# Kernel tuning notes

Measured on AMD Instinct MI355X. Metric: run time of the kernel, lower is better.

Reference implementation:

```python
import jax, jax.numpy as jnp
import numpy as np

N, E, D, H, C = 50000, 250000, 300, 4, 75  # nodes, edges, in_size=300, heads=4, out=75 (H*C=300)


def setup_inputs() -> dict:
    key = jax.random.key(0)
    ks = jax.random.split(key, 32)
    rn = lambda k, shape, s=0.05: jax.random.normal(k, shape, jnp.float32) * s
    inp = {}
    inp['x'] = rn(ks[0], (N, D), 1.0)
    inp['edge_index'] = jax.random.randint(ks[1], (2, E), 0, N, dtype=jnp.int32)
    inp['edge_attr'] = rn(ks[2], (E, 4), 1.0)
    inp['obj_normals'] = rn(ks[3], (N, 3), 1.0)
    # parameters (Linear stored as [in, out] so y = x @ W + b)
    inp['Wq'] = rn(ks[4], (D, H * C)); inp['bq'] = rn(ks[5], (H * C,))
    inp['Wk'] = rn(ks[6], (D, H * C)); inp['bk'] = rn(ks[7], (H * C,))
    inp['Wv'] = rn(ks[8], (D, H * C)); inp['bv'] = rn(ks[9], (H * C,))
    inp['We'] = rn(ks[10], (D, H * C))               # lin_edge, no bias
    inp['Wn'] = rn(ks[11], (3, D)); inp['bn'] = rn(ks[12], (D,))      # map_normal
    inp['Wxy'] = rn(ks[13], (2, D)); inp['bxy'] = rn(ks[14], (D,))    # map_xy_relative_coord
    inp['Wloc'] = rn(ks[15], (3 * D, D)); inp['bloc'] = rn(ks[16], (D,))  # map_back_edge_loc
    inp['Wobj'] = rn(ks[17], (2 * D, D)); inp['bobj'] = rn(ks[18], (D,))  # map_back_edge_obj
    inp['Wfus'] = rn(ks[19], (2 * D, D)); inp['bfus'] = rn(ks[20], (D,))  # hv_words_fusion
    inp['Wcls'] = rn(ks[21], (D, 5)); inp['bcls'] = rn(ks[22], (5,))      # horizontal_word_cls
    inp['Wskip'] = rn(ks[23], (D, H * C)); inp['bskip'] = rn(ks[24], (H * C,))  # lin_skip
    inp['vocab'] = rn(ks[25], (7, D), 1.0)  # spatial_vocab_we
    return inp


def reference(x, edge_index, edge_attr, obj_normals,
              Wq, bq, Wk, bk, Wv, bv, We, Wn, bn, Wxy, bxy,
              Wloc, bloc, Wobj, bobj, Wfus, bfus, Wcls, bcls,
              Wskip, bskip, vocab):
    src, dst = edge_index[0], edge_index[1]  # x_j = x[src], x_i = x[dst]
    x_i = x[dst]
    x_j = x[src]
    q = (x_i @ Wq + bq).reshape(E, H, C)
    k = (x_j @ Wk + bk).reshape(E, H, C)
    # vertical (top/bottom) word embeddings gated by edge_attr signs
    top = (edge_attr[:, 0] > 0).astype(x.dtype)[:, None] * vocab[0][None, :]
    bot = (edge_attr[:, 1] < 0).astype(x.dtype)[:, None] * vocab[1][None, :]
    vert = top + bot                                           # [E, D]
    # horizontal word probabilities from geometry + feature cues
    ni = obj_normals[dst] @ Wn + bn
    nj = obj_normals[src] @ Wn + bn
    xy = edge_attr[:, 2:4] @ Wxy + bxy
    loc = jnp.concatenate([xy, ni, nj], axis=1) @ Wloc + bloc
    obj = jnp.concatenate([x_i, x_j - x_i], axis=1) @ Wobj + bobj
    prob = jax.nn.softmax(jnp.tanh(obj + loc) @ Wcls + bcls, axis=1)   # [E, 5]
    horiz = prob @ vocab[2:7]                                  # [E, D]
    edge_word = jnp.concatenate([vert, horiz], axis=1) @ Wfus + bfus   # [E, D]
    ef = (edge_word @ We).reshape(E, H, C)                     # lin_edge
    k = k + ef
    # scaled dot-product attention with per-destination-node softmax
    alpha = (q * k).sum(-1) / jnp.asarray(np.sqrt(C), x.dtype)  # [E, H]
    m = jax.ops.segment_max(alpha, dst, num_segments=N)
    alpha = jnp.exp(alpha - m[dst])
    den = jax.ops.segment_sum(alpha, dst, num_segments=N)
    alpha = alpha / den[dst]
    v = (x_j @ Wv + bv).reshape(E, H, C) + ef
    msg = v * alpha[..., None]                                  # [E, H, C]
    out = jax.ops.segment_sum(msg, dst, num_segments=N).reshape(N, H * C)
    out = out + x @ Wskip + bskip                               # concat heads + root skip
    return out
```

## Files before the change

### kernel.cpp

```cpp
#include <hip/hip_runtime.h>
#include <hip/hip_bf16.h>
#include <math.h>

#define NDIM 300
#define KPAD 320
#define NREAL 1800
#define NPAD 1920

typedef __hip_bfloat16 bf16;
typedef __attribute__((ext_vector_type(8))) short short8;
typedef __attribute__((ext_vector_type(4))) float f32x4;

__device__ __forceinline__ void gl_lds16(const void* g, void* l) {
    __builtin_amdgcn_global_load_lds(
        (const __attribute__((address_space(1))) void*)g,
        (__attribute__((address_space(3))) void*)l, 16, 0, 0);
}

__global__ void small_pre(
    const float* __restrict__ Wn, const float* __restrict__ bn,
    const float* __restrict__ Wxy, const float* __restrict__ bxy,
    const float* __restrict__ Wloc, const float* __restrict__ bloc,
    const float* __restrict__ bobj,
    const float* __restrict__ Wfus,
    const float* __restrict__ vocab,
    float* __restrict__ Wn1, float* __restrict__ Wn2,
    float* __restrict__ Mxy, float* __restrict__ bgeo,
    float* __restrict__ vf5, float* __restrict__ t0, float* __restrict__ t1)
{
    int i = blockIdx.x * blockDim.x + threadIdx.x;
    if (i < 900) {
        int r = i / 300, c = i % 300;
        float s = 0.f;
        for (int k = 0; k < 300; k++) s += Wn[r*300+k] * Wloc[(300+k)*300+c];
        Wn1[i] = s;
    } else if (i < 1800) {
        int j = i - 900; int r = j/300, c = j%300;
        float s = 0.f;
        for (int k = 0; k < 300; k++) s += Wn[r*300+k] * Wloc[(600+k)*300+c];
        Wn2[j] = s;
    } else if (i < 2400) {
        int j = i - 1800; int r = j/300, c = j%300;
        float s = 0.f;
        for (int k = 0; k < 300; k++) s += Wxy[r*300+k] * Wloc[k*300+c];
        Mxy[j] = 2.f * s;
    } else if (i < 2700) {
        int c = i - 2400;
        float s = bloc[c] + bobj[c];
        for (int k = 0; k < 300; k++) s += bxy[k] * Wloc[k*300+c];
        for (int k = 0; k < 300; k++) s += bn[k] * (Wloc[(300+k)*300+c] + Wloc[(600+k)*300+c]);
        bgeo[c] = 2.f * s;
    } else if (i < 4200) {
        int j = i - 2700; int p = j/300, c = j%300;
        float s = 0.f;
        for (int k = 0; k < 300; k++) s += vocab[(2+p)*300+k] * Wfus[(300+k)*300+c];
        vf5[j] = s;
    } else if (i < 4500) {
        int c = i - 4200;
        float s = 0.f;
        for (int k = 0; k < 300; k++) s += vocab[k] * Wfus[k*300+c];
        t0[c] = s;
    } else if (i < 4800) {
        int c = i - 4500;
        float s = 0.f;
        for (int k = 0; k < 300; k++) s += vocab[300+k] * Wfus[k*300+c];
        t1[c] = s;
    }
}

__global__ void small_pre2(
    const float* __restrict__ We, const float* __restrict__ bfus,
    const float* __restrict__ vf5, const float* __restrict__ t0, const float* __restrict__ t1,
    const float* __restrict__ Wcls,
    float* __restrict__ E8, float* __restrict__ WclsT)
{
    int i = blockIdx.x * blockDim.x + threadIdx.x;
    if (i < 2400) {
        int r = i / 300, c = i % 300;
        const float* src;
        if (r == 0) src = t0;
        else if (r == 1) src = t1;
        else if (r == 7) src = bfus;
        else src = vf5 + (r - 2) * 300;
        float s = 0.f;
        for (int k = 0; k < 300; k++) s += src[k] * We[k*300+c];
        E8[i] = s;
    } else if (i < 3900) {
        int j = i - 2400; int cl = j / 300, c = j % 300;
        WclsT[cl * 300 + c] = Wcls[c * 5 + cl];
    }
}

__global__ void pack_w(
    const float* __restrict__ Wq, const float* __restrict__ Wk,
    const float* __restrict__ Wv, const float* __restrict__ Wskip,
    const float* __restrict__ Wobj,
    const float* __restrict__ Wn1, const float* __restrict__ Wn2,
    const float* __restrict__ bq, const float* __restrict__ bk,
    const float* __restrict__ bv, const float* __restrict__ bskip,
    bf16* __restrict__ WcatT, float* __restrict__ bcat)
{
    int i = blockIdx.x * blockDim.x + threadIdx.x;
    if (i < NREAL) {
        int seg = i / 300, jj = i % 300;
        float b = 0.f;
        if (seg == 0) b = bq[jj]; else if (seg == 1) b = bk[jj];
        else if (seg == 2) b = bv[jj]; else if (seg == 3) b = bskip[jj];
        bcat[i] = b;
    }
    if (i < NPAD * KPAD) {
        int c = i / KPAD, k = i % KPAD;
        float v = 0.f;
        if (c < NREAL) {
            int seg = c / 300, jj = c % 300;
            if (k < 300) {
                switch (seg) {
                    case 0: v = Wq[k*300+jj]; break;
                    case 1: v = Wk[k*300+jj]; break;
                    case 2: v = Wv[k*300+jj]; break;
                    case 3: v = Wskip[k*300+jj]; break;
                    case 4: v = Wobj[k*300+jj] - Wobj[(300+k)*300+jj]; break;
                    default: v = Wobj[(300+k)*300+jj]; break;
                }
            } else if (k < 303) {
                if (seg == 4) v = Wn1[(k-300)*300+jj];
                else if (seg == 5) v = Wn2[(k-300)*300+jj];
            }
            if (seg >= 4) v *= 2.f;
        }
        WcatT[i] = __float2bfloat16(v);
    }
}

__global__ void conv_xb(const float* __restrict__ X, const float* __restrict__ Nrm,
                        bf16* __restrict__ Xb, int M)
{
    int i = blockIdx.x * blockDim.x + threadIdx.x;
    int row = i / 40, c8 = i % 40;
    if (row >= M) return;
    int c0 = c8 * 8;
    union { bf16 h[8]; short8 s; } u;
    #pragma unroll
    for (int t = 0; t < 8; t++) {
        int c = c0 + t;
        float v = 0.f;
        if (c < 300)      v = X[(size_t)row * 300 + c];
        else if (c < 303) v = Nrm[(size_t)row * 3 + (c - 300)];
        u.h[t] = __float2bfloat16(v);
    }
    *(short8*)&Xb[(size_t)row * 320 + c0] = u.s;
}

__global__ __launch_bounds__(256) void qe8_k(
    const bf16* __restrict__ Q, const float* __restrict__ E8,
    float* __restrict__ QE8f, int N)
{
    __shared__ bf16 Qs[64 * 300];
    const int tid = threadIdx.x;
    const int n0 = blockIdx.x * 64;
    const int nrows = min(64, N - n0);
    const int ndw = nrows * 150;
    const uint* src = (const uint*)(Q + (size_t)n0 * 300);
    uint* dst = (uint*)Qs;
    for (int i = tid; i < ndw; i += 256) dst[i] = src[i];
    __syncthreads();
    const int w = tid >> 6, l = tid & 63;
    if (l >= nrows) return;
    float acc[8] = {0.f,0.f,0.f,0.f,0.f,0.f,0.f,0.f};
    const int cb = 75 * w;
    for (int cc = 0; cc < 75; cc++) {
        int c = cb + cc;
        float qv = __bfloat162float(Qs[l * 300 + c]);
        #pragma unroll
        for (int s = 0; s < 8; s++) acc[s] += qv * E8[s * 300 + c];
    }
    float* out = QE8f + (size_t)(n0 + l) * 32;
    #pragma unroll
    for (int s = 0; s < 8; s++) out[s * 4 + w] = acc[s];
}

__global__ void hist_k(const int* __restrict__ ei, int* __restrict__ deg, int E) {
    int e = blockIdx.x * blockDim.x + threadIdx.x;
    if (e < E) atomicAdd(&deg[ei[E + e]], 1);
}

__global__ __launch_bounds__(1024) void scan_local(
    const int* __restrict__ deg, int* __restrict__ off, int* __restrict__ bsum, int N)
{
    __shared__ int buf[1024];
    int i = blockIdx.x * 1024 + threadIdx.x;
    int v = (i < N) ? deg[i] : 0;
    buf[threadIdx.x] = v;
    __syncthreads();
    #pragma unroll
    for (int ofs = 1; ofs < 1024; ofs <<= 1) {
        int t = (threadIdx.x >= ofs) ? buf[threadIdx.x - ofs] : 0;
        __syncthreads();
        buf[threadIdx.x] += t;
        __syncthreads();
    }
    if (i < N) off[i] = buf[threadIdx.x] - v;
    if (threadIdx.x == 1023) bsum[blockIdx.x] = buf[1023];
}

__global__ __launch_bounds__(1024) void scan_bsum(
    const int* __restrict__ bsum, int* __restrict__ bexc, int nb)
{
    __shared__ int buf[1024];
    int v = (threadIdx.x < nb) ? bsum[threadIdx.x] : 0;
    buf[threadIdx.x] = v;
    __syncthreads();
    #pragma unroll
    for (int ofs = 1; ofs < 1024; ofs <<= 1) {
        int t = (threadIdx.x >= ofs) ? buf[threadIdx.x - ofs] : 0;
        __syncthreads();
        buf[threadIdx.x] += t;
        __syncthreads();
    }
    if (threadIdx.x < nb) bexc[threadIdx.x] = buf[threadIdx.x] - v;
}

__global__ void scan_add(int* __restrict__ off, int* __restrict__ cur,
                         const int* __restrict__ bexc, int N, int E)
{
    int i = blockIdx.x * blockDim.x + threadIdx.x;
    if (i < N) {
        int o = off[i] + bexc[i >> 10];
        off[i] = o; cur[i] = o;
    }
    if (i == 0) off[N] = E;
}

__global__ void scatter_k(const int* __restrict__ ei, const float* __restrict__ ea,
                          int* __restrict__ cur,
                          int* __restrict__ esrc, int* __restrict__ edst,
                          float* __restrict__ eas, int E) {
    int e = blockIdx.x * blockDim.x + threadIdx.x;
    if (e < E) {
        int s = ei[e];
        int d = ei[E + e];
        float4 a = *(const float4*)&ea[(size_t)e * 4];
        int p = atomicAdd(&cur[d], 1);
        esrc[p] = s;
        edst[p] = d;
        *(float4*)&eas[(size_t)p * 4] = a;
    }
}

__global__ __launch_bounds__(256) void gemm_mfma(
    const bf16* __restrict__ Xb,
    const bf16* __restrict__ Bt, const float* __restrict__ bcat,
    bf16* __restrict__ Q, bf16* __restrict__ Kf, bf16* __restrict__ V,
    float* __restrict__ Ot, bf16* __restrict__ Pi, bf16* __restrict__ Pj,
    int M)
{
    __shared__ __align__(16) bf16 As[2][128 * 32];
    __shared__ __align__(16) bf16 Bs[2][128 * 32];

    const int tid  = threadIdx.x;
    const int wave = tid >> 6;
    const int lane = tid & 63;
    const int r0 = blockIdx.y * 128;
    const int c0 = blockIdx.x * 128;
    const int wm = (wave >> 1) * 64;
    const int wn = (wave & 1) * 64;
    const int lr = lane & 15;
    const int lq = lane >> 4;

    f32x4 acc[4][4];
    #pragma unroll
    for (int j = 0; j < 4; j++)
        #pragma unroll
        for (int i = 0; i < 4; i++) acc[j][i] = (f32x4){0.f, 0.f, 0.f, 0.f};

    const int bcol_l = lane >> 2;
    const int bkp    = (lane & 3) * 8;

    auto stage = [&](int buf, int kb) {
        #pragma unroll
        for (int h = 0; h < 2; h++) {
            int tbase = h * 256 + wave * 64;
            int t = tbase + lane;
            int grow = min(r0 + (t >> 2), M - 1);
            gl_lds16(Xb + (size_t)grow * 320 + kb + (t & 3) * 8,
                     &As[buf][tbase * 8]);
        }
        #pragma unroll
        for (int h = 0; h < 2; h++) {
            int cloc = wave * 32 + h * 16;
            gl_lds16(Bt + (size_t)(c0 + cloc + bcol_l) * KPAD + kb + bkp,
                     &Bs[buf][cloc * 32]);
        }
    };

    stage(0, 0);
    #pragma unroll
    for (int it = 0; it < 10; it++) {
        __syncthreads();
        if (it < 9) stage((it + 1) & 1, (it + 1) * 32);
        const int b = it & 1;
        short8 af[4], bfr[4];
        #pragma unroll
        for (int i = 0; i < 4; i++)
            af[i] = *(const short8*)&As[b][(wm + i * 16 + lr) * 32 + lq * 8];
        #pragma unroll
        for (int j = 0; j < 4; j++)
            bfr[j] = *(const short8*)&Bs[b][(wn + j * 16 + lr) * 32 + lq * 8];
        #pragma unroll
        for (int j = 0; j < 4; j++)
            #pragma unroll
            for (int i = 0; i < 4; i++)
                acc[j][i] = __builtin_amdgcn_mfma_f32_16x16x32_bf16(
                    bfr[j], af[i], acc[j][i], 0, 0, 0);
    }

    #pragma unroll
    for (int j = 0; j < 4; j++) {
        int colb = c0 + wn + j * 16 + lq * 4;
        if (colb >= NREAL) continue;
        int seg = colb / 300, jj = colb - seg * 300;
        float4 bb = *(const float4*)&bcat[colb];
        #pragma unroll
        for (int i = 0; i < 4; i++) {
            int row = r0 + wm + i * 16 + lr;
            if (row >= M) continue;
            float v0 = acc[j][i][0] + bb.x;
            float v1 = acc[j][i][1] + bb.y;
            float v2 = acc[j][i][2] + bb.z;
            float v3 = acc[j][i][3] + bb.w;
            size_t idx = (size_t)row * 300 + jj;
            if (seg == 3) {
                *(float4*)&Ot[idx] = make_float4(v0, v1, v2, v3);
            } else {
                union { bf16 h[4]; uint2 u2; } p;
                p.h[0] = __float2bfloat16(v0); p.h[1] = __float2bfloat16(v1);
                p.h[2] = __float2bfloat16(v2); p.h[3] = __float2bfloat16(v3);
                bf16* base = (seg == 0) ? Q : (seg == 1) ? Kf : (seg == 2) ? V
                           : (seg == 4) ? Pi : Pj;
                *(uint2*)&base[idx] = p.u2;
            }
        }
    }
}

__global__ __launch_bounds__(256) void edge_alpha(
    const int* __restrict__ esrc, const int* __restrict__ edst,
    const float* __restrict__ eas,
    const bf16* __restrict__ Q, const bf16* __restrict__ Kf,
    const bf16* __restrict__ Pi, const bf16* __restrict__ Pj,
    const float* __restrict__ Mxy, const float* __restrict__ bgeo,
    const float* __restrict__ QE8f, const float* __restrict__ WclsT,
    const float* __restrict__ bcls,
    float* __restrict__ Aex, float* __restrict__ W8o,
    int E, int nwaves)
{
    __shared__ float red[4][20 * 68];
    __shared__ float res[4][20];
    const int wv   = threadIdx.x >> 6;
    const int lane = threadIdx.x & 63;
    float* __restrict__ rw = red[wv];
    float* __restrict__ rs = res[wv];
    const int gw  = blockIdx.x * 4 + wv;
    const int per = (E + nwaves - 1) / nwaves;
    const int t0  = gw * per;
    if (t0 >= E) return;
    const int t1 = min(t0 + per, E);

    float mx0[5], mx1[5], bg[5], wcl[5][5];
    #pragma unroll
    for (int r = 0; r < 5; r++) {
        int c = lane + 64 * r;
        bool ok = c < 300;
        mx0[r] = ok ? Mxy[c]       : 0.f;
        mx1[r] = ok ? Mxy[300 + c] : 0.f;
        bg[r]  = ok ? bgeo[c]      : 0.f;
        #pragma unroll
        for (int cl = 0; cl < 5; cl++)
            wcl[cl][r] = ok ? WclsT[cl * 300 + c] : 0.f;
    }
    float bc[5];
    #pragma unroll
    for (int cl = 0; cl < 5; cl++) bc[cl] = bcls[cl];
    const float isc = 0.11547005383792516f;

    for (int t = t0; t < t1; t += 2) {
        const int i0 = t;
        const int i1 = (t + 1 < t1) ? t + 1 : t;
        const int s20 = esrc[i0], s21 = esrc[i1];
        const int d20 = edst[i0], d21 = edst[i1];
        const float4 a40 = *(const float4*)&eas[(size_t)4 * i0];
        const float4 a41 = *(const float4*)&eas[(size_t)4 * i1];

        float prt[18];
        #pragma unroll
        for (int u = 0; u < 2; u++) {
            const int ss = u ? s21 : s20;
            const int dd = u ? d21 : d20;
            const float az = u ? a41.z : a40.z;
            const float aw = u ? a41.w : a40.w;
            const size_t sr = (size_t)ss * 300, dr = (size_t)dd * 300;
            float qv[5], kv[5], tt[5];
            #pragma unroll
            for (int r = 0; r < 5; r++) {
                int c = lane + 64 * r;
                bool ok = c < 300;
                float pi_ = ok ? __bfloat162float(Pi[dr + c]) : 0.f;
                float pj_ = ok ? __bfloat162float(Pj[sr + c]) : 0.f;
                qv[r] = ok ? __bfloat162float(Q [dr + c]) : 0.f;
                kv[r] = ok ? __bfloat162float(Kf[sr + c]) : 0.f;
                float v = pi_ + pj_ + az * mx0[r] + aw * mx1[r] + bg[r];
                tt[r] = fmaf(-2.f, __builtin_amdgcn_rcpf(1.f + __expf(v)), 1.f);
            }
            #pragma unroll
            for (int cl = 0; cl < 5; cl++)
                prt[u * 9 + cl] = tt[0]*wcl[cl][0] + tt[1]*wcl[cl][1] + tt[2]*wcl[cl][2]
                                + tt[3]*wcl[cl][3] + tt[4]*wcl[cl][4];
            float h0 = qv[0] * kv[0];
            float h3 = qv[4] * kv[4];
            float p1 = qv[1] * kv[1], p2 = qv[2] * kv[2], p3 = qv[3] * kv[3];
            float h1 = 0.f, h2 = 0.f;
            if (lane + 64  < 75)  h0 += p1; else h1 += p1;
            if (lane + 128 < 150) h1 += p2; else h2 += p2;
            if (lane + 192 < 225) h2 += p3; else h3 += p3;
            prt[u * 9 + 5] = h0; prt[u * 9 + 6] = h1;
            prt[u * 9 + 7] = h2; prt[u * 9 + 8] = h3;
        }
        #pragma unroll
        for (int v = 0; v < 18; v++) rw[v * 68 + lane] = prt[v];
        #pragma unroll
        for (int i = 0; i < 5; i++) {
            int v = 4 * i + (lane >> 4);
            const f32x4 q4 = *(const f32x4*)&rw[v * 68 + (lane & 15) * 4];
            float s = (q4[0] + q4[1]) + (q4[2] + q4[3]);
            s += __shfl_xor(s, 1, 64);
            s += __shfl_xor(s, 2, 64);
            s += __shfl_xor(s, 4, 64);
            s += __shfl_xor(s, 8, 64);
            if ((lane & 15) == 0 && v < 18) rs[v] = s;
        }
        {
            const int   u  = lane >> 5;
            const int   ub = u * 9;
            const float4 au = u ? a41 : a40;
            const int   dd = u ? d21 : d20;
            const int   tw = u ? i1 : i0;
            float lg0 = rs[ub+0] + bc[0], lg1 = rs[ub+1] + bc[1], lg2 = rs[ub+2] + bc[2];
            float lg3 = rs[ub+3] + bc[3], lg4 = rs[ub+4] + bc[4];
            float mxv = fmaxf(fmaxf(fmaxf(lg0, lg1), fmaxf(lg2, lg3)), lg4);
            float p0 = __expf(lg0 - mxv), p1 = __expf(lg1 - mxv), p2 = __expf(lg2 - mxv);
            float p3 = __expf(lg3 - mxv), p4 = __expf(lg4 - mxv);
            float pinv = __builtin_amdgcn_rcpf(p0 + p1 + p2 + p3 + p4);
            p0 *= pinv; p1 *= pinv; p2 *= pinv; p3 *= pinv; p4 *= pinv;
            float ct  = au.x > 0.f ? 1.f : 0.f;
            float cb_ = au.y < 0.f ? 1.f : 0.f;
            const f32x4* qe = (const f32x4*)(QE8f + (size_t)dd * 32);
            f32x4 addv = ct*qe[0] + cb_*qe[1] + p0*qe[2] + p1*qe[3]
                       + p2*qe[4] + p3*qe[5] + p4*qe[6] + qe[7];
            float ax0 = __expf((rs[ub+5] + addv[0]) * isc);
            float ax1 = __expf((rs[ub+6] + addv[1]) * isc);
            float ax2 = __expf((rs[ub+7] + addv[2]) * isc);
            float ax3 = __expf((rs[ub+8] + addv[3]) * isc);
            if ((lane & 31) == 0) {
                *(float4*)&Aex[(size_t)4*tw] = make_float4(ax0, ax1, ax2, ax3);
                *(float4*)&W8o[(size_t)8*tw]     = make_float4(ct, cb_, p0, p1);
                *(float4*)&W8o[(size_t)8*tw + 4] = make_float4(p2, p3, p4, 0.f);
            }
        }
    }
}

__global__ __launch_bounds__(256) void node_pv(
    const int* __restrict__ esrc, const bf16* __restrict__ V,
    const float* __restrict__ E8,
    const float* __restrict__ Aex, const float* __restrict__ W8o,
    const int* __restrict__ off,
    float* __restrict__ Ot, int N, int E)
{
    const int wid  = threadIdx.x >> 6;
    const int lane = threadIdx.x & 63;
    const int n = blockIdx.x * 4 + wid;
    if (n >= N) return;
    const int e0 = off[n], e1 = off[n + 1];
    if (e0 == e1) return;
    const size_t nrow = (size_t)n * 300;

    float e8r[8][5];
    #pragma unroll
    for (int rr = 0; rr < 8; rr++)
        #pragma unroll
        for (int r = 0; r < 5; r++) {
            int c = lane + 64 * r;
            e8r[rr][r] = (c < 300) ? E8[rr * 300 + c] : 0.f;
        }

    float macc[5] = {0.f, 0.f, 0.f, 0.f, 0.f};
    float den0 = 0.f, den1 = 0.f, den2 = 0.f, den3 = 0.f;

    auto body = [&](int t) {
        int s = esrc[t];
        float4 ax = *(const float4*)&Aex[(size_t)4 * t];
        float4 wa = *(const float4*)&W8o[(size_t)8 * t];
        float4 wb = *(const float4*)&W8o[(size_t)8 * t + 4];
        size_t sr = (size_t)s * 300;
        #pragma unroll
        for (int r = 0; r < 5; r++) {
            int c = lane + 64 * r;
            float vv = (c < 300) ? __bfloat162float(V[sr + c]) : 0.f;
            float efc = wa.x * e8r[0][r] + wa.y * e8r[1][r] + wa.z * e8r[2][r] + wa.w * e8r[3][r]
                      + wb.x * e8r[4][r] + wb.y * e8r[5][r] + wb.z * e8r[6][r] + e8r[7][r];
            float w = (r == 0) ? ax.x
                    : (r == 1) ? (c < 75  ? ax.x : ax.y)
                    : (r == 2) ? (c < 150 ? ax.y : ax.z)
                    : (r == 3) ? (c < 225 ? ax.z : ax.w)
                    : ax.w;
            macc[r] += w * (vv + efc);
        }
        den0 += ax.x; den1 += ax.y; den2 += ax.z; den3 += ax.w;
    };
    int t = e0;
    for (; t + 1 < e1; t += 2) { body(t); body(t + 1); }
    if (t < e1) body(t);

    const float rd0 = __builtin_amdgcn_rcpf(den0);
    const float rd1 = __builtin_amdgcn_rcpf(den1);
    const float rd2 = __builtin_amdgcn_rcpf(den2);
    const float rd3 = __builtin_amdgcn_rcpf(den3);
    #pragma unroll
    for (int r = 0; r < 5; r++) {
        int c = lane + 64 * r;
        if (c < 300) {
            float rd = (r == 0) ? rd0
                     : (r == 1) ? (c < 75  ? rd0 : rd1)
                     : (r == 2) ? (c < 150 ? rd1 : rd2)
                     : (r == 3) ? (c < 225 ? rd2 : rd3)
                     : rd3;
            Ot[nrow + c] += macc[r] * rd;
        }
    }
}

extern "C" void kernel_launch(void* const* d_in, const int* in_sizes, int n_in,
                              void* d_out, int out_size, void* d_ws, size_t ws_size,
                              hipStream_t stream)
{
    const float* x     = (const float*)d_in[0];
    const int*   ei    = (const int*)  d_in[1];
    const float* ea    = (const float*)d_in[2];
    const float* on    = (const float*)d_in[3];
    const float* Wq    = (const float*)d_in[4];
    const float* bq    = (const float*)d_in[5];
    const float* Wk    = (const float*)d_in[6];
    const float* bk    = (const float*)d_in[7];
    const float* Wv    = (const float*)d_in[8];
    const float* bv    = (const float*)d_in[9];
    const float* We    = (const float*)d_in[10];
    const float* Wn    = (const float*)d_in[11];
    const float* bn    = (const float*)d_in[12];
    const float* Wxy   = (const float*)d_in[13];
    const float* bxy   = (const float*)d_in[14];
    const float* Wloc  = (const float*)d_in[15];
    const float* bloc  = (const float*)d_in[16];
    const float* Wobj  = (const float*)d_in[17];
    const float* bobj  = (const float*)d_in[18];
    const float* Wfus  = (const float*)d_in[19];
    const float* bfus  = (const float*)d_in[20];
    const float* Wcls  = (const float*)d_in[21];
    const float* bcls  = (const float*)d_in[22];
    const float* Wskip = (const float*)d_in[23];
    const float* bskip = (const float*)d_in[24];
    const float* vocab = (const float*)d_in[25];

    const int N = in_sizes[0] / NDIM;
    const int E = in_sizes[1] / 2;

    const size_t nodeElems = (size_t)N * 300;
    const size_t wcatElems = (size_t)NPAD * KPAD;
    const size_t xbElems   = (size_t)N * 320;
    size_t xbBytes = xbElems * sizeof(bf16);
    const size_t ovlBytes = ((size_t)16 * E + (size_t)32 * N) * sizeof(float);
    if (ovlBytes > xbBytes) xbBytes = ovlBytes;

    const size_t f32Elems  = NREAL + 904 + 904 + 600 + 304 + 1504 + 304 + 304 + 2400 + 1504;
    const size_t intElems  = (size_t)N + (size_t)(N + 1) + (size_t)N
                           + (size_t)E + (size_t)E + 2048;
    size_t need = (5 * nodeElems + wcatElems) * sizeof(bf16) + xbBytes
                + f32Elems * sizeof(float) + intElems * sizeof(int);
    if (ws_size < need) return;

    bf16* wsh = (bf16*)d_ws;
    bf16* Qb    = wsh;                 bf16* Kb  = Qb + nodeElems;
    bf16* Vb    = Kb + nodeElems;      bf16* Pib = Vb + nodeElems;
    bf16* Pjb   = Pib + nodeElems;
    bf16* WcatT = Pjb + nodeElems;
    bf16* Xb    = WcatT + wcatElems;
    float* Aex  = (float*)Xb;
    float* W8o  = Aex + (size_t)4 * E;
    float* eas  = W8o + (size_t)8 * E;
    float* QE8f = eas + (size_t)4 * E;
    float* ws = (float*)((char*)Xb + xbBytes);
    size_t o = 0;
    float* bcat  = ws + o; o += NREAL;
    float* Wn1   = ws + o; o += 904;
    float* Wn2   = ws + o; o += 904;
    float* Mxyb  = ws + o; o += 600;
    float* bgeo  = ws + o; o += 304;
    float* vf5   = ws + o; o += 1504;
    float* t0b   = ws + o; o += 304;
    float* t1b   = ws + o; o += 304;
    float* E8b   = ws + o; o += 2400;
    float* WclsT = ws + o; o += 1504;
    int* ip = (int*)(ws + o);
    int* deg    = ip;             ip += N;
    int* offb   = ip;             ip += N + 1;
    int* curb   = ip;             ip += N;
    int* esrc   = ip;             ip += E;
    int* edst   = ip;             ip += E;
    int* bsum   = ip;             ip += 1024;
    int* bexc   = ip;             ip += 1024;
    (void)n_in; (void)out_size;

    hipMemsetAsync(deg, 0, (size_t)N * sizeof(int), stream);

    small_pre<<<19, 256, 0, stream>>>(Wn, bn, Wxy, bxy, Wloc, bloc, bobj, Wfus, vocab,
                                      Wn1, Wn2, Mxyb, bgeo, vf5, t0b, t1b);
    small_pre2<<<16, 256, 0, stream>>>(We, bfus, vf5, t0b, t1b, Wcls, E8b, WclsT);
    pack_w<<<(NPAD * KPAD + 255) / 256, 256, 0, stream>>>(
        Wq, Wk, Wv, Wskip, Wobj, Wn1, Wn2, bq, bk, bv, bskip, WcatT, bcat);
    conv_xb<<<((size_t)N * 40 + 255) / 256, 256, 0, stream>>>(x, on, Xb, N);

    const int ebk = (E + 255) / 256;
    hist_k<<<ebk, 256, 0, stream>>>(ei, deg, E);
    const int nbl = (N + 1023) / 1024;
    scan_local<<<nbl, 1024, 0, stream>>>(deg, offb, bsum, N);
    scan_bsum<<<1, 1024, 0, stream>>>(bsum, bexc, nbl);
    scan_add<<<(N + 255) / 256, 256, 0, stream>>>(offb, curb, bexc, N, E);

    dim3 g1(NPAD / 128, (N + 127) / 128);
    gemm_mfma<<<g1, 256, 0, stream>>>(Xb, WcatT, bcat,
                                      Qb, Kb, Vb, (float*)d_out, Pib, Pjb, N);

    scatter_k<<<ebk, 256, 0, stream>>>(ei, ea, curb, esrc, edst, eas, E);
    qe8_k<<<(N + 63) / 64, 256, 0, stream>>>(Qb, E8b, QE8f, N);

    const int eab = 2048;
    edge_alpha<<<eab, 256, 0, stream>>>(esrc, edst, eas, Qb, Kb, Pib, Pjb,
                                        Mxyb, bgeo, QE8f, WclsT, bcls,
                                        Aex, W8o, E, eab * 4);

    const int nb = (N + 3) / 4;
    node_pv<<<nb, 256, 0, stream>>>(esrc, Vb, E8b, Aex, W8o,
                                    offb, (float*)d_out, N, E);
}
```

Measured before the change: 734.4 us.

## Interleave Q/Pi and Pj/K columns, pack edge indices and per-edge outputs

The GEMM output columns are permuted so that Q and Pi share one interleaved buffer, and Pj and K share another. Each gather in edge_alpha then fetches both values with a single 32-bit load, and the Q/Pi row is reloaded only when the destination node changes between consecutive CSR-sorted edges. Edge src/dst are packed into int2, and the per-edge Aex/W8o outputs are merged into one 12-float record. The intent is to halve the gather transactions and cut redundant destination-row loads in the memory-bound edge kernel. In exchange, qe8_k now does strided LDS staging from the interleaved layout.

```diff
diff --git a/kernel.cpp b/kernel.cpp
--- a/kernel.cpp
+++ b/kernel.cpp
@@ -16,6 +16,9 @@
         (const __attribute__((address_space(1))) void*)g,
         (__attribute__((address_space(3))) void*)l, 16, 0, 0);
 }
+
+__device__ __forceinline__ float bflo(uint u) { return __uint_as_float(u << 16); }
+__device__ __forceinline__ float bfhi(uint u) { return __uint_as_float(u & 0xFFFF0000u); }
 
 __global__ void small_pre(
     const float* __restrict__ Wn, const float* __restrict__ bn,
@@ -102,17 +105,23 @@
 {
     int i = blockIdx.x * blockDim.x + threadIdx.x;
     if (i < NREAL) {
-        int seg = i / 300, jj = i % 300;
+        int c = i;
         float b = 0.f;
-        if (seg == 0) b = bq[jj]; else if (seg == 1) b = bk[jj];
-        else if (seg == 2) b = bv[jj]; else if (seg == 3) b = bskip[jj];
+        if (c < 600)       { if (!(c & 1)) b = bq[c >> 1]; }
+        else if (c < 1200) { int cc = c - 600; if (cc & 1) b = bk[cc >> 1]; }
+        else if (c < 1500) b = bv[c - 1200];
+        else               b = bskip[c - 1500];
         bcat[i] = b;
     }
     if (i < NPAD * KPAD) {
-        int c = i / KPAD, k = i % KPAD;
+        int cp = i / KPAD, k = i % KPAD;
         float v = 0.f;
-        if (c < NREAL) {
-            int seg = c / 300, jj = c % 300;
+        if (cp < NREAL) {
+            int seg, jj;
+            if (cp < 600)       { jj = cp >> 1; seg = (cp & 1) ? 4 : 0; }
+            else if (cp < 1200) { int cc = cp - 600; jj = cc >> 1; seg = (cc & 1) ? 1 : 5; }
+            else if (cp < 1500) { jj = cp - 1200; seg = 2; }
+            else                { jj = cp - 1500; seg = 3; }
             if (k < 300) {
                 switch (seg) {
                     case 0: v = Wq[k*300+jj]; break;
@@ -152,17 +161,19 @@
 }
 
 __global__ __launch_bounds__(256) void qe8_k(
-    const bf16* __restrict__ Q, const float* __restrict__ E8,
+    const bf16* __restrict__ QP, const float* __restrict__ E8,
     float* __restrict__ QE8f, int N)
 {
-    __shared__ bf16 Qs[64 * 300];
+    __shared__ unsigned short Qs[64 * 302];
     const int tid = threadIdx.x;
     const int n0 = blockIdx.x * 64;
     const int nrows = min(64, N - n0);
-    const int ndw = nrows * 150;
-    const uint* src = (const uint*)(Q + (size_t)n0 * 300);
-    uint* dst = (uint*)Qs;
-    for (int i = tid; i < ndw; i += 256) dst[i] = src[i];
+    const int nu = nrows * 300;
+    const uint* src = (const uint*)QP + (size_t)n0 * 300;
+    for (int i = tid; i < nu; i += 256) {
+        int rr = i / 300, cc = i - rr * 300;
+        Qs[rr * 302 + cc] = (unsigned short)src[i];
+    }
     __syncthreads();
     const int w = tid >> 6, l = tid & 63;
     if (l >= nrows) return;
@@ -170,7 +181,7 @@
     const int cb = 75 * w;
     for (int cc = 0; cc < 75; cc++) {
         int c = cb + cc;
-        float qv = __bfloat162float(Qs[l * 300 + c]);
+        float qv = __uint_as_float(((uint)Qs[l * 302 + c]) << 16);
         #pragma unroll
         for (int s = 0; s < 8; s++) acc[s] += qv * E8[s * 300 + c];
     }
@@ -233,16 +244,14 @@
 
 __global__ void scatter_k(const int* __restrict__ ei, const float* __restrict__ ea,
                           int* __restrict__ cur,
-                          int* __restrict__ esrc, int* __restrict__ edst,
-                          float* __restrict__ eas, int E) {
+                          int2* __restrict__ esd, float* __restrict__ eas, int E) {
     int e = blockIdx.x * blockDim.x + threadIdx.x;
     if (e < E) {
         int s = ei[e];
         int d = ei[E + e];
         float4 a = *(const float4*)&ea[(size_t)e * 4];
         int p = atomicAdd(&cur[d], 1);
-        esrc[p] = s;
-        edst[p] = d;
+        esd[p] = make_int2(s, d);
         *(float4*)&eas[(size_t)p * 4] = a;
     }
 }
@@ -250,9 +259,8 @@
 __global__ __launch_bounds__(256) void gemm_mfma(
     const bf16* __restrict__ Xb,
     const bf16* __restrict__ Bt, const float* __restrict__ bcat,
-    bf16* __restrict__ Q, bf16* __restrict__ Kf, bf16* __restrict__ V,
-    float* __restrict__ Ot, bf16* __restrict__ Pi, bf16* __restrict__ Pj,
-    int M)
+    bf16* __restrict__ QP, bf16* __restrict__ PK, bf16* __restrict__ V,
+    float* __restrict__ Ot, int M)
 {
     __shared__ __align__(16) bf16 As[2][128 * 32];
     __shared__ __align__(16) bf16 Bs[2][128 * 32];
@@ -318,7 +326,6 @@
     for (int j = 0; j < 4; j++) {
         int colb = c0 + wn + j * 16 + lq * 4;
         if (colb >= NREAL) continue;
-        int seg = colb / 300, jj = colb - seg * 300;
         float4 bb = *(const float4*)&bcat[colb];
         #pragma unroll
         for (int i = 0; i < 4; i++) {
@@ -328,33 +335,34 @@
             float v1 = acc[j][i][1] + bb.y;
             float v2 = acc[j][i][2] + bb.z;
             float v3 = acc[j][i][3] + bb.w;
-            size_t idx = (size_t)row * 300 + jj;
-            if (seg == 3) {
-                *(float4*)&Ot[idx] = make_float4(v0, v1, v2, v3);
-            } else {
+            if (colb < 1500) {
                 union { bf16 h[4]; uint2 u2; } p;
                 p.h[0] = __float2bfloat16(v0); p.h[1] = __float2bfloat16(v1);
                 p.h[2] = __float2bfloat16(v2); p.h[3] = __float2bfloat16(v3);
-                bf16* base = (seg == 0) ? Q : (seg == 1) ? Kf : (seg == 2) ? V
-                           : (seg == 4) ? Pi : Pj;
-                *(uint2*)&base[idx] = p.u2;
+                if (colb < 600)
+                    *(uint2*)&QP[(size_t)row * 600 + colb] = p.u2;
+                else if (colb < 1200)
+                    *(uint2*)&PK[(size_t)row * 600 + (colb - 600)] = p.u2;
+                else
+                    *(uint2*)&V[(size_t)row * 300 + (colb - 1200)] = p.u2;
+            } else {
+                *(float4*)&Ot[(size_t)row * 300 + (colb - 1500)] =
+                    make_float4(v0, v1, v2, v3);
             }
         }
     }
 }
 
 __global__ __launch_bounds__(256) void edge_alpha(
-    const int* __restrict__ esrc, const int* __restrict__ edst,
-    const float* __restrict__ eas,
-    const bf16* __restrict__ Q, const bf16* __restrict__ Kf,
-    const bf16* __restrict__ Pi, const bf16* __restrict__ Pj,
+    const int2* __restrict__ esd, const float* __restrict__ eas,
+    const bf16* __restrict__ QP, const bf16* __restrict__ PK,
     const float* __restrict__ Mxy, const float* __restrict__ bgeo,
     const float* __restrict__ QE8f, const float* __restrict__ WclsT,
     const float* __restrict__ bcls,
-    float* __restrict__ Aex, float* __restrict__ W8o,
+    float* __restrict__ AW,
     int E, int nwaves)
 {
-    __shared__ float red[4][20 * 68];
+    __shared__ __align__(16) float red[4][20 * 68];
     __shared__ float res[4][20];
     const int wv   = threadIdx.x >> 6;
     const int lane = threadIdx.x & 63;
@@ -365,66 +373,87 @@
     const int t0  = gw * per;
     if (t0 >= E) return;
     const int t1 = min(t0 + per, E);
+    const bool ok4 = lane < 44;
 
     float mx0[5], mx1[5], bg[5], wcl[5][5];
     #pragma unroll
-    for (int r = 0; r < 5; r++) {
+    for (int r = 0; r < 4; r++) {
         int c = lane + 64 * r;
-        bool ok = c < 300;
-        mx0[r] = ok ? Mxy[c]       : 0.f;
-        mx1[r] = ok ? Mxy[300 + c] : 0.f;
-        bg[r]  = ok ? bgeo[c]      : 0.f;
-        #pragma unroll
-        for (int cl = 0; cl < 5; cl++)
-            wcl[cl][r] = ok ? WclsT[cl * 300 + c] : 0.f;
+        mx0[r] = Mxy[c]; mx1[r] = Mxy[300 + c]; bg[r] = bgeo[c];
+        #pragma unroll
+        for (int cl = 0; cl < 5; cl++) wcl[cl][r] = WclsT[cl * 300 + c];
+    }
+    {
+        int c = lane + 256;
+        mx0[4] = ok4 ? Mxy[c] : 0.f;
+        mx1[4] = ok4 ? Mxy[300 + c] : 0.f;
+        bg[4]  = ok4 ? bgeo[c] : 0.f;
+        #pragma unroll
+        for (int cl = 0; cl < 5; cl++) wcl[cl][4] = ok4 ? WclsT[cl * 300 + c] : 0.f;
     }
     float bc[5];
     #pragma unroll
     for (int cl = 0; cl < 5; cl++) bc[cl] = bcls[cl];
     const float isc = 0.11547005383792516f;
+
+    const uint* QPu = (const uint*)QP;
+    const uint* PKu = (const uint*)PK;
+
+    int prev_d = -1;
+    float qv[5], pib[5];
+    float prt[18];
+
+    auto reload = [&](int dd) {
+        const uint* qr = QPu + (size_t)dd * 300 + lane;
+        #pragma unroll
+        for (int r = 0; r < 4; r++) {
+            uint uq = qr[64 * r];
+            qv[r] = bflo(uq); pib[r] = bfhi(uq) + bg[r];
+        }
+        uint uq = ok4 ? qr[256] : 0u;
+        qv[4] = bflo(uq); pib[4] = bfhi(uq) + bg[4];
+    };
+    auto compute = [&](const uint (&pk)[5], float az, float aw_, int ub) {
+        float tt[5], qk[5];
+        #pragma unroll
+        for (int r = 0; r < 5; r++) {
+            float pj = bflo(pk[r]), kf = bfhi(pk[r]);
+            float v = pib[r] + pj + az * mx0[r] + aw_ * mx1[r];
+            tt[r] = fmaf(-2.f, __builtin_amdgcn_rcpf(1.f + __expf(v)), 1.f);
+            qk[r] = qv[r] * kf;
+        }
+        #pragma unroll
+        for (int cl = 0; cl < 5; cl++)
+            prt[ub + cl] = tt[0]*wcl[cl][0] + tt[1]*wcl[cl][1] + tt[2]*wcl[cl][2]
+                         + tt[3]*wcl[cl][3] + tt[4]*wcl[cl][4];
+        float h0 = qk[0], h3 = qk[4], h1 = 0.f, h2 = 0.f;
+        if (lane < 11) h0 += qk[1]; else h1 += qk[1];
+        if (lane < 22) h1 += qk[2]; else h2 += qk[2];
+        if (lane < 33) h2 += qk[3]; else h3 += qk[3];
+        prt[ub+5] = h0; prt[ub+6] = h1; prt[ub+7] = h2; prt[ub+8] = h3;
+    };
 
     for (int t = t0; t < t1; t += 2) {
         const int i0 = t;
         const int i1 = (t + 1 < t1) ? t + 1 : t;
-        const int s20 = esrc[i0], s21 = esrc[i1];
-        const int d20 = edst[i0], d21 = edst[i1];
+        const int2 sd0 = esd[i0], sd1 = esd[i1];
         const float4 a40 = *(const float4*)&eas[(size_t)4 * i0];
         const float4 a41 = *(const float4*)&eas[(size_t)4 * i1];
 
-        float prt[18];
-        #pragma unroll
-        for (int u = 0; u < 2; u++) {
-            const int ss = u ? s21 : s20;
-            const int dd = u ? d21 : d20;
-            const float az = u ? a41.z : a40.z;
-            const float aw = u ? a41.w : a40.w;
-            const size_t sr = (size_t)ss * 300, dr = (size_t)dd * 300;
-            float qv[5], kv[5], tt[5];
-            #pragma unroll
-            for (int r = 0; r < 5; r++) {
-                int c = lane + 64 * r;
-                bool ok = c < 300;
-                float pi_ = ok ? __bfloat162float(Pi[dr + c]) : 0.f;
-                float pj_ = ok ? __bfloat162float(Pj[sr + c]) : 0.f;
-                qv[r] = ok ? __bfloat162float(Q [dr + c]) : 0.f;
-                kv[r] = ok ? __bfloat162float(Kf[sr + c]) : 0.f;
-                float v = pi_ + pj_ + az * mx0[r] + aw * mx1[r] + bg[r];
-                tt[r] = fmaf(-2.f, __builtin_amdgcn_rcpf(1.f + __expf(v)), 1.f);
-            }
-            #pragma unroll
-            for (int cl = 0; cl < 5; cl++)
-                prt[u * 9 + cl] = tt[0]*wcl[cl][0] + tt[1]*wcl[cl][1] + tt[2]*wcl[cl][2]
-                                + tt[3]*wcl[cl][3] + tt[4]*wcl[cl][4];
-            float h0 = qv[0] * kv[0];
-            float h3 = qv[4] * kv[4];
-            float p1 = qv[1] * kv[1], p2 = qv[2] * kv[2], p3 = qv[3] * kv[3];
-            float h1 = 0.f, h2 = 0.f;
-            if (lane + 64  < 75)  h0 += p1; else h1 += p1;
-            if (lane + 128 < 150) h1 += p2; else h2 += p2;
-            if (lane + 192 < 225) h2 += p3; else h3 += p3;
-            prt[u * 9 + 5] = h0; prt[u * 9 + 6] = h1;
-            prt[u * 9 + 7] = h2; prt[u * 9 + 8] = h3;
-        }
+        uint pk0[5], pk1[5];
+        const uint* p0r = PKu + (size_t)sd0.x * 300 + lane;
+        const uint* p1r = PKu + (size_t)sd1.x * 300 + lane;
+        #pragma unroll
+        for (int r = 0; r < 4; r++) { pk0[r] = p0r[64 * r]; pk1[r] = p1r[64 * r]; }
+        pk0[4] = ok4 ? p0r[256] : 0u;
+        pk1[4] = ok4 ? p1r[256] : 0u;
+
+        if (sd0.y != prev_d) reload(sd0.y);
+        compute(pk0, a40.z, a40.w, 0);
+        if (sd1.y != sd0.y) reload(sd1.y);
+        compute(pk1, a41.z, a41.w, 9);
+        prev_d = sd1.y;
+
         #pragma unroll
         for (int v = 0; v < 18; v++) rw[v * 68 + lane] = prt[v];
         #pragma unroll
@@ -439,11 +468,11 @@
             if ((lane & 15) == 0 && v < 18) rs[v] = s;
         }
         {
-            const int   u  = lane >> 5;
-            const int   ub = u * 9;
+            const int    u  = lane >> 5;
+            const int    ub = u * 9;
             const float4 au = u ? a41 : a40;
-            const int   dd = u ? d21 : d20;
-            const int   tw = u ? i1 : i0;
+            const int    dd = u ? sd1.y : sd0.y;
+            const int    tw = u ? i1 : i0;
             float lg0 = rs[ub+0] + bc[0], lg1 = rs[ub+1] + bc[1], lg2 = rs[ub+2] + bc[2];
             float lg3 = rs[ub+3] + bc[3], lg4 = rs[ub+4] + bc[4];
             float mxv = fmaxf(fmaxf(fmaxf(lg0, lg1), fmaxf(lg2, lg3)), lg4);
@@ -461,20 +490,20 @@
             float ax2 = __expf((rs[ub+7] + addv[2]) * isc);
             float ax3 = __expf((rs[ub+8] + addv[3]) * isc);
             if ((lane & 31) == 0) {
-                *(float4*)&Aex[(size_t)4*tw] = make_float4(ax0, ax1, ax2, ax3);
-                *(float4*)&W8o[(size_t)8*tw]     = make_float4(ct, cb_, p0, p1);
-                *(float4*)&W8o[(size_t)8*tw + 4] = make_float4(p2, p3, p4, 0.f);
+                float* awp = AW + (size_t)12 * tw;
+                *(float4*)(awp)     = make_float4(ax0, ax1, ax2, ax3);
+                *(float4*)(awp + 4) = make_float4(ct, cb_, p0, p1);
+                *(float4*)(awp + 8) = make_float4(p2, p3, p4, 0.f);
             }
         }
     }
 }
 
 __global__ __launch_bounds__(256) void node_pv(
-    const int* __restrict__ esrc, const bf16* __restrict__ V,
-    const float* __restrict__ E8,
-    const float* __restrict__ Aex, const float* __restrict__ W8o,
+    const int2* __restrict__ esd, const bf16* __restrict__ V,
+    const float* __restrict__ E8, const float* __restrict__ AW,
     const int* __restrict__ off,
-    float* __restrict__ Ot, int N, int E)
+    float* __restrict__ Ot, int N)
 {
     const int wid  = threadIdx.x >> 6;
     const int lane = threadIdx.x & 63;
@@ -483,35 +512,36 @@
     const int e0 = off[n], e1 = off[n + 1];
     if (e0 == e1) return;
     const size_t nrow = (size_t)n * 300;
+    const bool ok4 = lane < 44;
 
     float e8r[8][5];
     #pragma unroll
-    for (int rr = 0; rr < 8; rr++)
-        #pragma unroll
-        for (int r = 0; r < 5; r++) {
-            int c = lane + 64 * r;
-            e8r[rr][r] = (c < 300) ? E8[rr * 300 + c] : 0.f;
-        }
+    for (int rr = 0; rr < 8; rr++) {
+        #pragma unroll
+        for (int r = 0; r < 4; r++) e8r[rr][r] = E8[rr * 300 + lane + 64 * r];
+        e8r[rr][4] = ok4 ? E8[rr * 300 + lane + 256] : 0.f;
+    }
 
     float macc[5] = {0.f, 0.f, 0.f, 0.f, 0.f};
     float den0 = 0.f, den1 = 0.f, den2 = 0.f, den3 = 0.f;
 
     auto body = [&](int t) {
-        int s = esrc[t];
-        float4 ax = *(const float4*)&Aex[(size_t)4 * t];
-        float4 wa = *(const float4*)&W8o[(size_t)8 * t];
-        float4 wb = *(const float4*)&W8o[(size_t)8 * t + 4];
-        size_t sr = (size_t)s * 300;
+        int s = esd[t].x;
+        const float* awp = AW + (size_t)12 * t;
+        float4 ax = *(const float4*)(awp);
+        float4 wa = *(const float4*)(awp + 4);
+        float4 wb = *(const float4*)(awp + 8);
+        const bf16* vr = V + (size_t)s * 300 + lane;
         #pragma unroll
         for (int r = 0; r < 5; r++) {
-            int c = lane + 64 * r;
-            float vv = (c < 300) ? __bfloat162float(V[sr + c]) : 0.f;
+            float vv = (r < 4) ? __bfloat162float(vr[64 * r])
+                               : (ok4 ? __bfloat162float(vr[256]) : 0.f);
             float efc = wa.x * e8r[0][r] + wa.y * e8r[1][r] + wa.z * e8r[2][r] + wa.w * e8r[3][r]
                       + wb.x * e8r[4][r] + wb.y * e8r[5][r] + wb.z * e8r[6][r] + e8r[7][r];
             float w = (r == 0) ? ax.x
-                    : (r == 1) ? (c < 75  ? ax.x : ax.y)
-                    : (r == 2) ? (c < 150 ? ax.y : ax.z)
-                    : (r == 3) ? (c < 225 ? ax.z : ax.w)
+                    : (r == 1) ? (lane < 11 ? ax.x : ax.y)
+                    : (r == 2) ? (lane < 22 ? ax.y : ax.z)
+                    : (r == 3) ? (lane < 33 ? ax.z : ax.w)
                     : ax.w;
             macc[r] += w * (vv + efc);
         }
@@ -530,9 +560,9 @@
         int c = lane + 64 * r;
         if (c < 300) {
             float rd = (r == 0) ? rd0
-                     : (r == 1) ? (c < 75  ? rd0 : rd1)
-                     : (r == 2) ? (c < 150 ? rd1 : rd2)
-                     : (r == 3) ? (c < 225 ? rd2 : rd3)
+                     : (r == 1) ? (lane < 11 ? rd0 : rd1)
+                     : (r == 2) ? (lane < 22 ? rd1 : rd2)
+                     : (r == 3) ? (lane < 33 ? rd2 : rd3)
                      : rd3;
             Ot[nrow + c] += macc[r] * rd;
         }
@@ -582,20 +612,19 @@
 
     const size_t f32Elems  = NREAL + 904 + 904 + 600 + 304 + 1504 + 304 + 304 + 2400 + 1504;
     const size_t intElems  = (size_t)N + (size_t)(N + 1) + (size_t)N
-                           + (size_t)E + (size_t)E + 2048;
+                           + (size_t)2 * E + 2048;
     size_t need = (5 * nodeElems + wcatElems) * sizeof(bf16) + xbBytes
                 + f32Elems * sizeof(float) + intElems * sizeof(int);
     if (ws_size < need) return;
 
     bf16* wsh = (bf16*)d_ws;
-    bf16* Qb    = wsh;                 bf16* Kb  = Qb + nodeElems;
-    bf16* Vb    = Kb + nodeElems;      bf16* Pib = Vb + nodeElems;
-    bf16* Pjb   = Pib + nodeElems;
-    bf16* WcatT = Pjb + nodeElems;
+    bf16* QPb   = wsh;
+    bf16* PKb   = QPb + (size_t)2 * nodeElems;
+    bf16* Vb    = PKb + (size_t)2 * nodeElems;
+    bf16* WcatT = Vb + nodeElems;
     bf16* Xb    = WcatT + wcatElems;
-    float* Aex  = (float*)Xb;
-    float* W8o  = Aex + (size_t)4 * E;
-    float* eas  = W8o + (size_t)8 * E;
+    float* AW   = (float*)Xb;
+    float* eas  = AW + (size_t)12 * E;
     float* QE8f = eas + (size_t)4 * E;
     float* ws = (float*)((char*)Xb + xbBytes);
     size_t o = 0;
@@ -613,8 +642,7 @@
     int* deg    = ip;             ip += N;
     int* offb   = ip;             ip += N + 1;
     int* curb   = ip;             ip += N;
-    int* esrc   = ip;             ip += E;
-    int* edst   = ip;             ip += E;
+    int2* esd   = (int2*)ip;      ip += (size_t)2 * E;
     int* bsum   = ip;             ip += 1024;
     int* bexc   = ip;             ip += 1024;
     (void)n_in; (void)out_size;
@@ -637,17 +665,17 @@
 
     dim3 g1(NPAD / 128, (N + 127) / 128);
     gemm_mfma<<<g1, 256, 0, stream>>>(Xb, WcatT, bcat,
-                                      Qb, Kb, Vb, (float*)d_out, Pib, Pjb, N);
-
-    scatter_k<<<ebk, 256, 0, stream>>>(ei, ea, curb, esrc, edst, eas, E);
-    qe8_k<<<(N + 63) / 64, 256, 0, stream>>>(Qb, E8b, QE8f, N);
+                                      QPb, PKb, Vb, (float*)d_out, N);
+
+    scatter_k<<<ebk, 256, 0, stream>>>(ei, ea, curb, esd, eas, E);
+    qe8_k<<<(N + 63) / 64, 256, 0, stream>>>(QPb, E8b, QE8f, N);
 
     const int eab = 2048;
-    edge_alpha<<<eab, 256, 0, stream>>>(esrc, edst, eas, Qb, Kb, Pib, Pjb,
+    edge_alpha<<<eab, 256, 0, stream>>>(esd, eas, QPb, PKb,
                                         Mxyb, bgeo, QE8f, WclsT, bcls,
-                                        Aex, W8o, E, eab * 4);
+                                        AW, E, eab * 4);
 
     const int nb = (N + 3) / 4;
-    node_pv<<<nb, 256, 0, stream>>>(esrc, Vb, E8b, Aex, W8o,
-                                    offb, (float*)d_out, N, E);
-}
+    node_pv<<<nb, 256, 0, stream>>>(esd, Vb, E8b, AW,
+                                    offb, (float*)d_out, N);
+}
```

Result: faster. 674.9 us (-8.1%).
